# Performance work log

Measured on AMD Instinct MI355X. Metric: run time of the kernel, lower is better.

## Reference

```python
import jax, jax.numpy as jnp
import numpy as np

MIN = 1e-15   # norm / denominator clamp (as in Poincare ball impl)
EPS = 1e-7    # artanh input clamp (fp32-safe version of 1-1e-15)
C = 1.0       # curvature (c_in == c_out == 1.0)
B, N, D = 1, 1024, 64


def _artanh(y):
    y = jnp.clip(y, -1.0 + EPS, 1.0 - EPS)
    return 0.5 * (jnp.log1p(y) - jnp.log1p(-y))


def _norm(v):
    return jnp.maximum(jnp.linalg.norm(v, axis=-1, keepdims=True), MIN)


def expmap0(u, c):
    sqc = jnp.sqrt(c)
    n = _norm(u)
    return jnp.tanh(sqc * n) * u / (sqc * n)


def logmap0(p, c):
    sqc = jnp.sqrt(c)
    n = _norm(p)
    return _artanh(sqc * n) * p / (sqc * n)


def mobius_add(x, y, c):
    x2 = jnp.sum(x * x, -1, keepdims=True)
    y2 = jnp.sum(y * y, -1, keepdims=True)
    xy = jnp.sum(x * y, -1, keepdims=True)
    num = (1.0 + 2.0 * c * xy + c * y2) * x + (1.0 - c * x2) * y
    den = 1.0 + 2.0 * c * xy + c * c * x2 * y2
    return num / jnp.maximum(den, MIN)


def mobius_matvec(m, x, c):
    # m: [out, in], x: [B, N, in]
    sqc = jnp.sqrt(c)
    xn = _norm(x)
    mx = jnp.einsum('bnd,ed->bne', x, m)
    mxn = _norm(mx)
    res = jnp.tanh(mxn / xn * _artanh(sqc * xn)) * mx / (mxn * sqc)
    cond = jnp.all(mx == 0.0, axis=-1, keepdims=True)
    return jnp.where(cond, jnp.zeros_like(res), res)


def logmap(p1, p2, c):
    # tangent vector at p1 pointing to p2 (broadcasts)
    sqc = jnp.sqrt(c)
    sub = mobius_add(-p1, p2, c)
    sn = _norm(sub)
    lam = 2.0 / jnp.maximum(1.0 - c * jnp.sum(p1 * p1, -1, keepdims=True), MIN)
    return 2.0 / (sqc * lam) * _artanh(sqc * sn) * sub / sn


def expmap(u, p, c):
    # exp map of tangent u at point p (call order matches torch code: expmap(x, support_t))
    sqc = jnp.sqrt(c)
    un = _norm(u)
    lam = 2.0 / jnp.maximum(1.0 - c * jnp.sum(p * p, -1, keepdims=True), MIN)
    second = jnp.tanh(sqc / 2.0 * lam * un) * u / (sqc * un)
    return mobius_add(p, second, c)


def setup_inputs() -> dict:
    key = jax.random.key(0)
    k1, k2, k3, k4, k5 = jax.random.split(key, 5)
    # hyperbolic points: expmap0 of small tangent vectors -> valid Poincare-ball points
    x = expmap0(0.1 * jax.random.normal(k1, (B, N, D), jnp.float32), C)
    adj = (jax.random.uniform(k2, (B, N, N)) < 0.05).astype(jnp.float32)
    # xavier_uniform with gain sqrt(2): bound = sqrt(2)*sqrt(6/(D+D))
    bound = np.sqrt(2.0) * np.sqrt(6.0 / (D + D))
    weight = jax.random.uniform(k3, (D, D), jnp.float32, -bound, bound)
    bias = 0.01 * jax.random.normal(k4, (D,), jnp.float32)
    kw, kb = jax.random.split(k5)
    ab = np.sqrt(6.0 / (2 * D + 1))
    att_w = jax.random.uniform(kw, (1, 2 * D), jnp.float32, -ab, ab)
    att_b = 0.01 * jax.random.normal(kb, (1,), jnp.float32)
    return {"x": x, "adj": adj, "weight": weight, "bias": bias,
            "att_w": att_w, "att_b": att_b}


def reference(x, adj, weight, bias, att_w, att_b):
    c = C
    # ---- HypLinear (dropout=0 / eval mode) ----
    h = mobius_matvec(weight, x, c)
    hyp_bias = expmap0(bias[None, :], c)          # proj_tan0 is identity on the ball
    h = mobius_add(h, hyp_bias, c)                # [B,N,D]
    # ---- HypAgg: use_att + local_agg ----
    h_tan = logmap0(h, c)                         # [B,N,D]
    # pairwise logmap: tangent_i[j] = logmap(h_i, h_j)  -> [B,N,N,D]
    local_tan = logmap(h[:, :, None, :], h[:, None, :, :], c)
    # DenseAtt on tangent features
    left = jnp.broadcast_to(h_tan[:, :, None, :], (B, N, N, D))
    right = jnp.broadcast_to(h_tan[:, None, :, :], (B, N, N, D))
    cat = jnp.concatenate([left, right], axis=-1)          # [B,N,N,2D]
    logits = jnp.einsum('bijk,ok->bij', cat, att_w) + att_b[0]
    att = jax.nn.sigmoid(logits) * adj                     # [B,N,N]
    support = jnp.sum(att[..., None] * local_tan, axis=2)  # [B,N,D]
    out = expmap(h, support, c)                            # faithful arg order: (x, support_t)
    # ---- HypAct ----
    t = jax.nn.relu(logmap0(out, c))
    return expmap0(t, c)
```

## Files before the change

### kernel.cpp

```cpp
#include <hip/hip_runtime.h>
#include <hip/hip_bf16.h>

#define NODES 1024
#define DIM   64
#define MINV  1e-15f
#define EPSV  1e-7f
#define WPAD  66
#define HPAD  66
#define CH    64

__device__ __forceinline__ float artanh_f(float y) {
    y = fminf(fmaxf(y, -1.f + EPSV), 1.f - EPSV);
    return 0.5f * (log1pf(y) - log1pf(-y));
}

__device__ __forceinline__ float waveReduceSum(float v) {
#pragma unroll
    for (int m = 1; m < 64; m <<= 1) v += __shfl_xor(v, m, 64);
    return v;
}

__global__ __launch_bounds__(256) void prep_kernel(
    const float* __restrict__ x,
    const float* __restrict__ weight,
    const float* __restrict__ bias,
    const float* __restrict__ att_w,
    float* __restrict__ H, float* __restrict__ X2,
    float* __restrict__ L, float* __restrict__ R)
{
    __shared__ float sx[4][DIM];
    __shared__ float Wl[DIM][WPAD];
    const int tid = threadIdx.x;
    const int wv  = tid >> 6;
    const int t   = tid & 63;
    const int i   = blockIdx.x * 4 + wv;

#pragma unroll
    for (int p = 0; p < 4; ++p) {
        const int k = p * 1024 + tid * 4;
        const float4 w4 = *reinterpret_cast<const float4*>(weight + k);
        const int r = k >> 6, c = k & 63;
        Wl[r][c + 0] = w4.x; Wl[r][c + 1] = w4.y;
        Wl[r][c + 2] = w4.z; Wl[r][c + 3] = w4.w;
    }

    const float xd = x[i * DIM + t];
    sx[wv][t] = xd;
    __syncthreads();

    const float xn = fmaxf(sqrtf(waveReduceSum(xd * xd)), MINV);

    float mx = 0.f;
    const float* sxr = sx[wv];
#pragma unroll
    for (int d = 0; d < DIM; d += 2) {
        const float2 w2 = *reinterpret_cast<const float2*>(&Wl[t][d]);
        mx = fmaf(sxr[d + 0], w2.x, mx);
        mx = fmaf(sxr[d + 1], w2.y, mx);
    }

    const float mxn = fmaxf(sqrtf(waveReduceSum(mx * mx)), MINV);
    const float res = tanhf(mxn / xn * artanh_f(xn)) * mx / mxn;

    const float bd = bias[t];
    const float bn = fmaxf(sqrtf(waveReduceSum(bd * bd)), MINV);
    const float hb = tanhf(bn) * bd / bn;

    const float y2  = waveReduceSum(hb * hb);
    const float x2r = waveReduceSum(res * res);
    const float xy  = waveReduceSum(res * hb);
    const float num = (1.f + 2.f * xy + y2) * res + (1.f - x2r) * hb;
    const float den = fmaxf(1.f + 2.f * xy + x2r * y2, MINV);
    const float h   = num / den;

    const float x2 = waveReduceSum(h * h);
    H[i * DIM + t] = h;

    const float n  = fmaxf(sqrtf(x2), MINV);
    const float ht = artanh_f(n) / n * h;
    const float Li = waveReduceSum(ht * att_w[t]);
    const float Ri = waveReduceSum(ht * att_w[DIM + t]);

    if (t == 0) { X2[i] = x2; L[i] = Li; R[i] = Ri; }
}

__global__ __launch_bounds__(256) void agg_kernel(
    const float* __restrict__ H, const float* __restrict__ X2,
    const float* __restrict__ L, const float* __restrict__ R,
    const float* __restrict__ adj,
    const float* __restrict__ att_b,
    float* __restrict__ out)
{
    __shared__ float shi[DIM];
    __shared__ float Hl[CH][HPAD];
    __shared__ float f_arr[CH];
    __shared__ int   slist[NODES];
    __shared__ int   wbase[4];
    __shared__ float svred[4][DIM];
    __shared__ float s0red[4];

    const int i   = blockIdx.x;
    const int tid = threadIdx.x;
    const int wv  = tid >> 6;
    const int ln  = tid & 63;
    const int grp = tid >> 4;
    const int gl  = tid & 15;
    const int d0  = gl * 4;

    if (tid < DIM) shi[tid] = H[i * DIM + tid];

    const float4 a4 = *reinterpret_cast<const float4*>(adj + i * NODES + tid * 4);
    const int c0 = (a4.x != 0.f), c1 = (a4.y != 0.f), c2 = (a4.z != 0.f), c3 = (a4.w != 0.f);
    const int cntv = c0 + c1 + c2 + c3;

    int pfx = cntv;
#pragma unroll
    for (int d = 1; d < 64; d <<= 1) {
        const int tsh = __shfl_up(pfx, d, 64);
        if (ln >= d) pfx += tsh;
    }
    if (ln == 63) wbase[wv] = pfx;
    __syncthreads();

    int base = 0;
#pragma unroll
    for (int w = 0; w < 4; ++w) if (w < wv) base += wbase[w];
    int pos = base + pfx - cntv;
    const int j0 = tid * 4;
    if (c0) slist[pos++] = j0 + 0;
    if (c1) slist[pos++] = j0 + 1;
    if (c2) slist[pos++] = j0 + 2;
    if (c3) slist[pos++] = j0 + 3;
    __syncthreads();
    const int cnt = wbase[0] + wbase[1] + wbase[2] + wbase[3];

    const float x2i   = X2[i];
    const float Li    = L[i];
    const float Bi    = 1.f - x2i;
    const float coefi = fmaxf(Bi, MINV);
    const float attb  = att_b[0];

    float4 vacc = make_float4(0.f, 0.f, 0.f, 0.f);
    float  s0   = 0.f;

    for (int cb = 0; cb < cnt; cb += CH) {
        const int m = min(CH, cnt - cb);

        {
            const int il = tid >> 4;
#pragma unroll
            for (int p = 0; p < 4; ++p) {
                const int ii = il + p * 16;
                if (ii < m) {
                    const int j = slist[cb + ii];
                    const float4 hv = *reinterpret_cast<const float4*>(H + j * DIM + d0);
                    float* dst = &Hl[ii][d0];
                    dst[0] = hv.x; dst[1] = hv.y; dst[2] = hv.z; dst[3] = hv.w;
                }
            }
        }
        __syncthreads();

        if (tid < m) {
            const int j = slist[cb + tid];
            float dot = 0.f;
            const float* hr = Hl[tid];
#pragma unroll
            for (int d = 0; d < DIM; d += 2) {
                const float2 h2 = *reinterpret_cast<const float2*>(&hr[d]);
                dot = fmaf(shi[d + 0], h2.x, dot);
                dot = fmaf(shi[d + 1], h2.y, dot);
            }

            const float y2  = X2[j];
            const float A   = 1.f - 2.f * dot + y2;
            const float den = fmaxf(1.f - 2.f * dot + x2i * y2, MINV);
            const float q   = fmaxf(A * A * x2i - 2.f * A * Bi * dot + Bi * Bi * y2, 0.f);
            const float sn  = fmaxf(sqrtf(q) / den, MINV);
            const float ratio = artanh_f(sn) / sn;

            const float logit = Li + R[j] + attb;
            const float sig   = 1.f / (1.f + expf(-logit));
            const float f     = sig * coefi * ratio / den;

            f_arr[tid] = f;
            s0 += f * A;
        }
        __syncthreads();

        for (int il = grp; il < m; il += 16) {
            const float fv = f_arr[il];
            const float* hr = &Hl[il][d0];
            vacc.x = fmaf(fv, hr[0], vacc.x);
            vacc.y = fmaf(fv, hr[1], vacc.y);
            vacc.z = fmaf(fv, hr[2], vacc.z);
            vacc.w = fmaf(fv, hr[3], vacc.w);
        }
        __syncthreads();
    }

    vacc.x += __shfl_xor(vacc.x, 16, 64); vacc.x += __shfl_xor(vacc.x, 32, 64);
    vacc.y += __shfl_xor(vacc.y, 16, 64); vacc.y += __shfl_xor(vacc.y, 32, 64);
    vacc.z += __shfl_xor(vacc.z, 16, 64); vacc.z += __shfl_xor(vacc.z, 32, 64);
    vacc.w += __shfl_xor(vacc.w, 16, 64); vacc.w += __shfl_xor(vacc.w, 32, 64);
    s0 = waveReduceSum(s0);

    if (ln < 16) {
        svred[wv][ln * 4 + 0] = vacc.x;
        svred[wv][ln * 4 + 1] = vacc.y;
        svred[wv][ln * 4 + 2] = vacc.z;
        svred[wv][ln * 4 + 3] = vacc.w;
    }
    if (ln == 0) s0red[wv] = s0;
    __syncthreads();

    if (tid < DIM) {
        const float svec = svred[0][tid] + svred[1][tid] + svred[2][tid] + svred[3][tid];
        const float s0t  = s0red[0] + s0red[1] + s0red[2] + s0red[3];
        const float hd   = shi[tid];
        const float sup  = -s0t * hd + Bi * svec;

        const float s2     = waveReduceSum(sup * sup);
        const float coef_s = fmaxf(1.f - s2, MINV);
        const float un     = fmaxf(sqrtf(x2i), MINV);
        const float tt     = tanhf(un / coef_s);
        const float sec    = tt * hd / un;

        const float y2s = waveReduceSum(sec * sec);
        const float xy  = waveReduceSum(sup * sec);
        const float num = (1.f + 2.f * xy + y2s) * sup + (1.f - s2) * sec;
        const float den = fmaxf(1.f + 2.f * xy + s2 * y2s, MINV);
        const float od  = num / den;

        const float on   = fmaxf(sqrtf(waveReduceSum(od * od)), MINV);
        const float tanv = artanh_f(on) / on * od;
        const float tv   = fmaxf(tanv, 0.f);
        const float tn   = fmaxf(sqrtf(waveReduceSum(tv * tv)), MINV);
        const float fin  = tanhf(tn) / tn * tv;

        out[i * DIM + tid] = fin;
    }
}

extern "C" void kernel_launch(void* const* d_in, const int* in_sizes, int n_in,
                              void* d_out, int out_size, void* d_ws, size_t ws_size,
                              hipStream_t stream) {
    const float* x      = (const float*)d_in[0];
    const float* adj    = (const float*)d_in[1];
    const float* weight = (const float*)d_in[2];
    const float* bias   = (const float*)d_in[3];
    const float* att_w  = (const float*)d_in[4];
    const float* att_b  = (const float*)d_in[5];

    float* ws = (float*)d_ws;
    float* H  = ws;
    float* X2 = ws + NODES * DIM;
    float* Lb = X2 + NODES;
    float* Rb = Lb + NODES;

    prep_kernel<<<NODES / 4, 256, 0, stream>>>(x, weight, bias, att_w, H, X2, Lb, Rb);
    agg_kernel<<<NODES, 256, 0, stream>>>(H, X2, Lb, Rb, adj, att_b,
                                          (float*)d_out);
}
```

Baseline: 18.58 us.

## Restructure aggregation kernel as single-wave blocks without LDS tiling

```diff
diff --git a/kernel.cpp b/kernel.cpp
--- a/kernel.cpp
+++ b/kernel.cpp
@@ -6,8 +6,6 @@
 #define MINV  1e-15f
 #define EPSV  1e-7f
 #define WPAD  66
-#define HPAD  66
-#define CH    64
 
 __device__ __forceinline__ float artanh_f(float y) {
     y = fminf(fmaxf(y, -1.f + EPSV), 1.f - EPSV);
@@ -18,6 +16,15 @@
 #pragma unroll
     for (int m = 1; m < 64; m <<= 1) v += __shfl_xor(v, m, 64);
     return v;
+}
+
+__device__ __forceinline__ void waveReduceSum2(float& a, float& b) {
+#pragma unroll
+    for (int m = 1; m < 64; m <<= 1) {
+        const float ta = __shfl_xor(a, m, 64);
+        const float tb = __shfl_xor(b, m, 64);
+        a += ta; b += tb;
+    }
 }
 
 __global__ __launch_bounds__(256) void prep_kernel(
@@ -84,55 +91,49 @@
     if (t == 0) { X2[i] = x2; L[i] = Li; R[i] = Ri; }
 }
 
-__global__ __launch_bounds__(256) void agg_kernel(
+__global__ __launch_bounds__(64) void agg_kernel(
     const float* __restrict__ H, const float* __restrict__ X2,
     const float* __restrict__ L, const float* __restrict__ R,
     const float* __restrict__ adj,
     const float* __restrict__ att_b,
     float* __restrict__ out)
 {
-    __shared__ float shi[DIM];
-    __shared__ float Hl[CH][HPAD];
-    __shared__ float f_arr[CH];
+    __shared__ float sh[DIM];
+    __shared__ float f_arr[NODES];
     __shared__ int   slist[NODES];
-    __shared__ int   wbase[4];
-    __shared__ float svred[4][DIM];
-    __shared__ float s0red[4];
-
-    const int i   = blockIdx.x;
-    const int tid = threadIdx.x;
-    const int wv  = tid >> 6;
-    const int ln  = tid & 63;
-    const int grp = tid >> 4;
-    const int gl  = tid & 15;
-    const int d0  = gl * 4;
-
-    if (tid < DIM) shi[tid] = H[i * DIM + tid];
-
-    const float4 a4 = *reinterpret_cast<const float4*>(adj + i * NODES + tid * 4);
-    const int c0 = (a4.x != 0.f), c1 = (a4.y != 0.f), c2 = (a4.z != 0.f), c3 = (a4.w != 0.f);
-    const int cntv = c0 + c1 + c2 + c3;
-
+
+    const int i  = blockIdx.x;
+    const int ln = threadIdx.x;
+
+    const float hd = H[i * DIM + ln];
+    sh[ln] = hd;
+
+    unsigned m16 = 0;
+    {
+        const float4* arow = reinterpret_cast<const float4*>(adj + i * NODES + ln * 16);
+#pragma unroll
+        for (int q = 0; q < 4; ++q) {
+            const float4 a = arow[q];
+            m16 |= (a.x != 0.f ? 1u : 0u) << (q * 4 + 0);
+            m16 |= (a.y != 0.f ? 1u : 0u) << (q * 4 + 1);
+            m16 |= (a.z != 0.f ? 1u : 0u) << (q * 4 + 2);
+            m16 |= (a.w != 0.f ? 1u : 0u) << (q * 4 + 3);
+        }
+    }
+    const int cntv = __popc(m16);
     int pfx = cntv;
 #pragma unroll
     for (int d = 1; d < 64; d <<= 1) {
-        const int tsh = __shfl_up(pfx, d, 64);
-        if (ln >= d) pfx += tsh;
-    }
-    if (ln == 63) wbase[wv] = pfx;
+        const int t = __shfl_up(pfx, d, 64);
+        if (ln >= d) pfx += t;
+    }
+    const int cnt = __shfl(pfx, 63, 64);
+    int pos = pfx - cntv;
+    const int jb = ln * 16;
+#pragma unroll
+    for (int q = 0; q < 16; ++q)
+        if (m16 & (1u << q)) slist[pos++] = jb + q;
     __syncthreads();
-
-    int base = 0;
-#pragma unroll
-    for (int w = 0; w < 4; ++w) if (w < wv) base += wbase[w];
-    int pos = base + pfx - cntv;
-    const int j0 = tid * 4;
-    if (c0) slist[pos++] = j0 + 0;
-    if (c1) slist[pos++] = j0 + 1;
-    if (c2) slist[pos++] = j0 + 2;
-    if (c3) slist[pos++] = j0 + 3;
-    __syncthreads();
-    const int cnt = wbase[0] + wbase[1] + wbase[2] + wbase[3];
 
     const float x2i   = X2[i];
     const float Li    = L[i];
@@ -140,106 +141,69 @@
     const float coefi = fmaxf(Bi, MINV);
     const float attb  = att_b[0];
 
-    float4 vacc = make_float4(0.f, 0.f, 0.f, 0.f);
-    float  s0   = 0.f;
-
-    for (int cb = 0; cb < cnt; cb += CH) {
-        const int m = min(CH, cnt - cb);
-
-        {
-            const int il = tid >> 4;
-#pragma unroll
-            for (int p = 0; p < 4; ++p) {
-                const int ii = il + p * 16;
-                if (ii < m) {
-                    const int j = slist[cb + ii];
-                    const float4 hv = *reinterpret_cast<const float4*>(H + j * DIM + d0);
-                    float* dst = &Hl[ii][d0];
-                    dst[0] = hv.x; dst[1] = hv.y; dst[2] = hv.z; dst[3] = hv.w;
-                }
-            }
+    float s0 = 0.f;
+    for (int k = ln; k < cnt; k += 64) {
+        const int j  = slist[k];
+        const float y2 = X2[j];
+        const float Rj = R[j];
+
+        float dot = 0.f;
+        const float* hj = H + j * DIM;
+#pragma unroll
+        for (int dd = 0; dd < DIM; dd += 4) {
+            const float4 h4 = *reinterpret_cast<const float4*>(hj + dd);
+            const float4 s4 = *reinterpret_cast<const float4*>(&sh[dd]);
+            dot = fmaf(h4.x, s4.x, dot);
+            dot = fmaf(h4.y, s4.y, dot);
+            dot = fmaf(h4.z, s4.z, dot);
+            dot = fmaf(h4.w, s4.w, dot);
         }
-        __syncthreads();
-
-        if (tid < m) {
-            const int j = slist[cb + tid];
-            float dot = 0.f;
-            const float* hr = Hl[tid];
-#pragma unroll
-            for (int d = 0; d < DIM; d += 2) {
-                const float2 h2 = *reinterpret_cast<const float2*>(&hr[d]);
-                dot = fmaf(shi[d + 0], h2.x, dot);
-                dot = fmaf(shi[d + 1], h2.y, dot);
-            }
-
-            const float y2  = X2[j];
-            const float A   = 1.f - 2.f * dot + y2;
-            const float den = fmaxf(1.f - 2.f * dot + x2i * y2, MINV);
-            const float q   = fmaxf(A * A * x2i - 2.f * A * Bi * dot + Bi * Bi * y2, 0.f);
-            const float sn  = fmaxf(sqrtf(q) / den, MINV);
-            const float ratio = artanh_f(sn) / sn;
-
-            const float logit = Li + R[j] + attb;
-            const float sig   = 1.f / (1.f + expf(-logit));
-            const float f     = sig * coefi * ratio / den;
-
-            f_arr[tid] = f;
-            s0 += f * A;
-        }
-        __syncthreads();
-
-        for (int il = grp; il < m; il += 16) {
-            const float fv = f_arr[il];
-            const float* hr = &Hl[il][d0];
-            vacc.x = fmaf(fv, hr[0], vacc.x);
-            vacc.y = fmaf(fv, hr[1], vacc.y);
-            vacc.z = fmaf(fv, hr[2], vacc.z);
-            vacc.w = fmaf(fv, hr[3], vacc.w);
-        }
-        __syncthreads();
-    }
-
-    vacc.x += __shfl_xor(vacc.x, 16, 64); vacc.x += __shfl_xor(vacc.x, 32, 64);
-    vacc.y += __shfl_xor(vacc.y, 16, 64); vacc.y += __shfl_xor(vacc.y, 32, 64);
-    vacc.z += __shfl_xor(vacc.z, 16, 64); vacc.z += __shfl_xor(vacc.z, 32, 64);
-    vacc.w += __shfl_xor(vacc.w, 16, 64); vacc.w += __shfl_xor(vacc.w, 32, 64);
+
+        const float A   = 1.f - 2.f * dot + y2;
+        const float den = fmaxf(1.f - 2.f * dot + x2i * y2, MINV);
+        const float q   = fmaxf(A * A * x2i - 2.f * A * Bi * dot + Bi * Bi * y2, 0.f);
+        const float sn  = fmaxf(sqrtf(q) / den, MINV);
+        const float ratio = artanh_f(sn) / sn;
+
+        const float sig = 1.f / (1.f + expf(-(Li + Rj + attb)));
+        const float f   = sig * coefi * ratio / den;
+
+        f_arr[k] = f;
+        s0 += f * A;
+    }
+    __syncthreads();
+
+    float sv = 0.f;
+#pragma unroll 4
+    for (int k = 0; k < cnt; ++k) {
+        const int j   = slist[k];
+        const float f = f_arr[k];
+        sv = fmaf(f, H[j * DIM + ln], sv);
+    }
+
     s0 = waveReduceSum(s0);
-
-    if (ln < 16) {
-        svred[wv][ln * 4 + 0] = vacc.x;
-        svred[wv][ln * 4 + 1] = vacc.y;
-        svred[wv][ln * 4 + 2] = vacc.z;
-        svred[wv][ln * 4 + 3] = vacc.w;
-    }
-    if (ln == 0) s0red[wv] = s0;
-    __syncthreads();
-
-    if (tid < DIM) {
-        const float svec = svred[0][tid] + svred[1][tid] + svred[2][tid] + svred[3][tid];
-        const float s0t  = s0red[0] + s0red[1] + s0red[2] + s0red[3];
-        const float hd   = shi[tid];
-        const float sup  = -s0t * hd + Bi * svec;
-
-        const float s2     = waveReduceSum(sup * sup);
-        const float coef_s = fmaxf(1.f - s2, MINV);
-        const float un     = fmaxf(sqrtf(x2i), MINV);
-        const float tt     = tanhf(un / coef_s);
-        const float sec    = tt * hd / un;
-
-        const float y2s = waveReduceSum(sec * sec);
-        const float xy  = waveReduceSum(sup * sec);
-        const float num = (1.f + 2.f * xy + y2s) * sup + (1.f - s2) * sec;
-        const float den = fmaxf(1.f + 2.f * xy + s2 * y2s, MINV);
-        const float od  = num / den;
-
-        const float on   = fmaxf(sqrtf(waveReduceSum(od * od)), MINV);
-        const float tanv = artanh_f(on) / on * od;
-        const float tv   = fmaxf(tanv, 0.f);
-        const float tn   = fmaxf(sqrtf(waveReduceSum(tv * tv)), MINV);
-        const float fin  = tanhf(tn) / tn * tv;
-
-        out[i * DIM + tid] = fin;
-    }
+    const float sup = -s0 * hd + Bi * sv;
+
+    const float s2     = waveReduceSum(sup * sup);
+    const float coef_s = fmaxf(1.f - s2, MINV);
+    const float un     = fmaxf(sqrtf(x2i), MINV);
+    const float tt     = tanhf(un / coef_s);
+    const float sec    = tt * hd / un;
+
+    float y2s = sec * sec;
+    float xy  = sup * sec;
+    waveReduceSum2(y2s, xy);
+    const float num = (1.f + 2.f * xy + y2s) * sup + (1.f - s2) * sec;
+    const float den = fmaxf(1.f + 2.f * xy + s2 * y2s, MINV);
+    const float od  = num / den;
+
+    const float on   = fmaxf(sqrtf(waveReduceSum(od * od)), MINV);
+    const float tanv = artanh_f(on) / on * od;
+    const float tv   = fmaxf(tanv, 0.f);
+    const float tn   = fmaxf(sqrtf(waveReduceSum(tv * tv)), MINV);
+    const float fin  = tanhf(tn) / tn * tv;
+
+    out[i * DIM + ln] = fin;
 }
 
 extern "C" void kernel_launch(void* const* d_in, const int* in_sizes, int n_in,
@@ -259,6 +223,6 @@
     float* Rb = Lb + NODES;
 
     prep_kernel<<<NODES / 4, 256, 0, stream>>>(x, weight, bias, att_w, H, X2, Lb, Rb);
-    agg_kernel<<<NODES, 256, 0, stream>>>(H, X2, Lb, Rb, adj, att_b,
-                                          (float*)d_out);
-}
+    agg_kernel<<<NODES, 64, 0, stream>>>(H, X2, Lb, Rb, adj, att_b,
+                                         (float*)d_out);
+}
```

Result: slower. 20.81 us (+12.0%).

## Fuse prep and aggregation kernels with a software grid barrier

Applied to the files above, without the earlier changes.

```diff
diff --git a/kernel.cpp b/kernel.cpp
--- a/kernel.cpp
+++ b/kernel.cpp
@@ -8,6 +8,7 @@
 #define WPAD  66
 #define HPAD  66
 #define CH    64
+#define GRID  256
 
 __device__ __forceinline__ float artanh_f(float y) {
     y = fminf(fmaxf(y, -1.f + EPSV), 1.f - EPSV);
@@ -19,78 +20,38 @@
     for (int m = 1; m < 64; m <<= 1) v += __shfl_xor(v, m, 64);
     return v;
 }
-
-__global__ __launch_bounds__(256) void prep_kernel(
+__device__ __forceinline__ void waveReduceSum2(float& a, float& b) {
+#pragma unroll
+    for (int m = 1; m < 64; m <<= 1) {
+        const float ta = __shfl_xor(a, m, 64);
+        const float tb = __shfl_xor(b, m, 64);
+        a += ta; b += tb;
+    }
+}
+__device__ __forceinline__ void waveReduceSum3(float& a, float& b, float& c) {
+#pragma unroll
+    for (int m = 1; m < 64; m <<= 1) {
+        const float ta = __shfl_xor(a, m, 64);
+        const float tb = __shfl_xor(b, m, 64);
+        const float tc = __shfl_xor(c, m, 64);
+        a += ta; b += tb; c += tc;
+    }
+}
+
+__global__ __launch_bounds__(256) void fused_kernel(
     const float* __restrict__ x,
+    const float* __restrict__ adj,
     const float* __restrict__ weight,
     const float* __restrict__ bias,
     const float* __restrict__ att_w,
+    const float* __restrict__ att_b,
     float* __restrict__ H, float* __restrict__ X2,
-    float* __restrict__ L, float* __restrict__ R)
+    float* __restrict__ L, float* __restrict__ R,
+    unsigned* __restrict__ bar,
+    float* __restrict__ out)
 {
     __shared__ float sx[4][DIM];
     __shared__ float Wl[DIM][WPAD];
-    const int tid = threadIdx.x;
-    const int wv  = tid >> 6;
-    const int t   = tid & 63;
-    const int i   = blockIdx.x * 4 + wv;
-
-#pragma unroll
-    for (int p = 0; p < 4; ++p) {
-        const int k = p * 1024 + tid * 4;
-        const float4 w4 = *reinterpret_cast<const float4*>(weight + k);
-        const int r = k >> 6, c = k & 63;
-        Wl[r][c + 0] = w4.x; Wl[r][c + 1] = w4.y;
-        Wl[r][c + 2] = w4.z; Wl[r][c + 3] = w4.w;
-    }
-
-    const float xd = x[i * DIM + t];
-    sx[wv][t] = xd;
-    __syncthreads();
-
-    const float xn = fmaxf(sqrtf(waveReduceSum(xd * xd)), MINV);
-
-    float mx = 0.f;
-    const float* sxr = sx[wv];
-#pragma unroll
-    for (int d = 0; d < DIM; d += 2) {
-        const float2 w2 = *reinterpret_cast<const float2*>(&Wl[t][d]);
-        mx = fmaf(sxr[d + 0], w2.x, mx);
-        mx = fmaf(sxr[d + 1], w2.y, mx);
-    }
-
-    const float mxn = fmaxf(sqrtf(waveReduceSum(mx * mx)), MINV);
-    const float res = tanhf(mxn / xn * artanh_f(xn)) * mx / mxn;
-
-    const float bd = bias[t];
-    const float bn = fmaxf(sqrtf(waveReduceSum(bd * bd)), MINV);
-    const float hb = tanhf(bn) * bd / bn;
-
-    const float y2  = waveReduceSum(hb * hb);
-    const float x2r = waveReduceSum(res * res);
-    const float xy  = waveReduceSum(res * hb);
-    const float num = (1.f + 2.f * xy + y2) * res + (1.f - x2r) * hb;
-    const float den = fmaxf(1.f + 2.f * xy + x2r * y2, MINV);
-    const float h   = num / den;
-
-    const float x2 = waveReduceSum(h * h);
-    H[i * DIM + t] = h;
-
-    const float n  = fmaxf(sqrtf(x2), MINV);
-    const float ht = artanh_f(n) / n * h;
-    const float Li = waveReduceSum(ht * att_w[t]);
-    const float Ri = waveReduceSum(ht * att_w[DIM + t]);
-
-    if (t == 0) { X2[i] = x2; L[i] = Li; R[i] = Ri; }
-}
-
-__global__ __launch_bounds__(256) void agg_kernel(
-    const float* __restrict__ H, const float* __restrict__ X2,
-    const float* __restrict__ L, const float* __restrict__ R,
-    const float* __restrict__ adj,
-    const float* __restrict__ att_b,
-    float* __restrict__ out)
-{
     __shared__ float shi[DIM];
     __shared__ float Hl[CH][HPAD];
     __shared__ float f_arr[CH];
@@ -99,146 +60,213 @@
     __shared__ float svred[4][DIM];
     __shared__ float s0red[4];
 
-    const int i   = blockIdx.x;
     const int tid = threadIdx.x;
     const int wv  = tid >> 6;
-    const int ln  = tid & 63;
+    const int t   = tid & 63;
+
+    {
+        const int i = blockIdx.x * 4 + wv;
+
+#pragma unroll
+        for (int p = 0; p < 4; ++p) {
+            const int k = p * 1024 + tid * 4;
+            const float4 w4 = *reinterpret_cast<const float4*>(weight + k);
+            const int r = k >> 6, c = k & 63;
+            Wl[r][c + 0] = w4.x; Wl[r][c + 1] = w4.y;
+            Wl[r][c + 2] = w4.z; Wl[r][c + 3] = w4.w;
+        }
+
+        const float xd = x[i * DIM + t];
+        sx[wv][t] = xd;
+        __syncthreads();
+
+        const float xn = fmaxf(sqrtf(waveReduceSum(xd * xd)), MINV);
+
+        float mx = 0.f;
+        const float* sxr = sx[wv];
+#pragma unroll
+        for (int d = 0; d < DIM; d += 2) {
+            const float2 w2 = *reinterpret_cast<const float2*>(&Wl[t][d]);
+            mx = fmaf(sxr[d + 0], w2.x, mx);
+            mx = fmaf(sxr[d + 1], w2.y, mx);
+        }
+
+        const float bd = bias[t];
+        float mxn2 = mx * mx, bn2 = bd * bd;
+        waveReduceSum2(mxn2, bn2);
+        const float mxn = fmaxf(sqrtf(mxn2), MINV);
+        const float res = tanhf(mxn / xn * artanh_f(xn)) * mx / mxn;
+        const float bn  = fmaxf(sqrtf(bn2), MINV);
+        const float hb  = tanhf(bn) * bd / bn;
+
+        float y2 = hb * hb, x2r = res * res, xy = res * hb;
+        waveReduceSum3(y2, x2r, xy);
+        const float num = (1.f + 2.f * xy + y2) * res + (1.f - x2r) * hb;
+        const float den = fmaxf(1.f + 2.f * xy + x2r * y2, MINV);
+        const float h   = num / den;
+
+        const float x2 = waveReduceSum(h * h);
+        H[i * DIM + t] = h;
+
+        const float n  = fmaxf(sqrtf(x2), MINV);
+        const float ht = artanh_f(n) / n * h;
+        float Li = ht * att_w[t], Ri = ht * att_w[DIM + t];
+        waveReduceSum2(Li, Ri);
+
+        if (t == 0) { X2[i] = x2; L[i] = Li; R[i] = Ri; }
+    }
+
+    __syncthreads();
+    if (tid == 0) {
+        __threadfence();
+        atomicAdd(bar, 1u);
+        unsigned spins = 0;
+        while (atomicAdd(bar, 0u) < GRID && ++spins < 100000000u)
+            __builtin_amdgcn_s_sleep(2);
+        __threadfence();
+    }
+    __syncthreads();
+
     const int grp = tid >> 4;
     const int gl  = tid & 15;
     const int d0  = gl * 4;
-
-    if (tid < DIM) shi[tid] = H[i * DIM + tid];
-
-    const float4 a4 = *reinterpret_cast<const float4*>(adj + i * NODES + tid * 4);
-    const int c0 = (a4.x != 0.f), c1 = (a4.y != 0.f), c2 = (a4.z != 0.f), c3 = (a4.w != 0.f);
-    const int cntv = c0 + c1 + c2 + c3;
-
-    int pfx = cntv;
-#pragma unroll
-    for (int d = 1; d < 64; d <<= 1) {
-        const int tsh = __shfl_up(pfx, d, 64);
-        if (ln >= d) pfx += tsh;
-    }
-    if (ln == 63) wbase[wv] = pfx;
-    __syncthreads();
-
-    int base = 0;
-#pragma unroll
-    for (int w = 0; w < 4; ++w) if (w < wv) base += wbase[w];
-    int pos = base + pfx - cntv;
-    const int j0 = tid * 4;
-    if (c0) slist[pos++] = j0 + 0;
-    if (c1) slist[pos++] = j0 + 1;
-    if (c2) slist[pos++] = j0 + 2;
-    if (c3) slist[pos++] = j0 + 3;
-    __syncthreads();
-    const int cnt = wbase[0] + wbase[1] + wbase[2] + wbase[3];
-
-    const float x2i   = X2[i];
-    const float Li    = L[i];
-    const float Bi    = 1.f - x2i;
-    const float coefi = fmaxf(Bi, MINV);
-    const float attb  = att_b[0];
-
-    float4 vacc = make_float4(0.f, 0.f, 0.f, 0.f);
-    float  s0   = 0.f;
-
-    for (int cb = 0; cb < cnt; cb += CH) {
-        const int m = min(CH, cnt - cb);
-
-        {
-            const int il = tid >> 4;
-#pragma unroll
-            for (int p = 0; p < 4; ++p) {
-                const int ii = il + p * 16;
-                if (ii < m) {
-                    const int j = slist[cb + ii];
-                    const float4 hv = *reinterpret_cast<const float4*>(H + j * DIM + d0);
-                    float* dst = &Hl[ii][d0];
-                    dst[0] = hv.x; dst[1] = hv.y; dst[2] = hv.z; dst[3] = hv.w;
+    const float attb = att_b[0];
+
+    for (int r = 0; r < 4; ++r) {
+        const int i = blockIdx.x * 4 + r;
+        __syncthreads();
+
+        if (tid < DIM) shi[tid] = H[i * DIM + tid];
+
+        const float4 a4 = *reinterpret_cast<const float4*>(adj + i * NODES + tid * 4);
+        const int c0 = (a4.x != 0.f), c1 = (a4.y != 0.f), c2 = (a4.z != 0.f), c3 = (a4.w != 0.f);
+        const int cntv = c0 + c1 + c2 + c3;
+
+        int pfx = cntv;
+#pragma unroll
+        for (int d = 1; d < 64; d <<= 1) {
+            const int tsh = __shfl_up(pfx, d, 64);
+            if (t >= d) pfx += tsh;
+        }
+        if (t == 63) wbase[wv] = pfx;
+        __syncthreads();
+
+        int base = 0;
+#pragma unroll
+        for (int w = 0; w < 4; ++w) if (w < wv) base += wbase[w];
+        int pos = base + pfx - cntv;
+        const int j0 = tid * 4;
+        if (c0) slist[pos++] = j0 + 0;
+        if (c1) slist[pos++] = j0 + 1;
+        if (c2) slist[pos++] = j0 + 2;
+        if (c3) slist[pos++] = j0 + 3;
+        __syncthreads();
+        const int cnt = wbase[0] + wbase[1] + wbase[2] + wbase[3];
+
+        const float x2i   = X2[i];
+        const float Li    = L[i];
+        const float Bi    = 1.f - x2i;
+        const float coefi = fmaxf(Bi, MINV);
+
+        float4 vacc = make_float4(0.f, 0.f, 0.f, 0.f);
+        float  s0   = 0.f;
+
+        for (int cb = 0; cb < cnt; cb += CH) {
+            const int m = min(CH, cnt - cb);
+
+            {
+                const int il = tid >> 4;
+#pragma unroll
+                for (int p = 0; p < 4; ++p) {
+                    const int ii = il + p * 16;
+                    if (ii < m) {
+                        const int j = slist[cb + ii];
+                        const float4 hv = *reinterpret_cast<const float4*>(H + j * DIM + d0);
+                        float* dst = &Hl[ii][d0];
+                        dst[0] = hv.x; dst[1] = hv.y; dst[2] = hv.z; dst[3] = hv.w;
+                    }
                 }
             }
-        }
-        __syncthreads();
-
-        if (tid < m) {
-            const int j = slist[cb + tid];
-            float dot = 0.f;
-            const float* hr = Hl[tid];
-#pragma unroll
-            for (int d = 0; d < DIM; d += 2) {
-                const float2 h2 = *reinterpret_cast<const float2*>(&hr[d]);
-                dot = fmaf(shi[d + 0], h2.x, dot);
-                dot = fmaf(shi[d + 1], h2.y, dot);
+            __syncthreads();
+
+            if (tid < m) {
+                const int j = slist[cb + tid];
+                float dot = 0.f;
+                const float* hr = Hl[tid];
+#pragma unroll
+                for (int d = 0; d < DIM; d += 2) {
+                    const float2 h2 = *reinterpret_cast<const float2*>(&hr[d]);
+                    dot = fmaf(shi[d + 0], h2.x, dot);
+                    dot = fmaf(shi[d + 1], h2.y, dot);
+                }
+
+                const float y2  = X2[j];
+                const float A   = 1.f - 2.f * dot + y2;
+                const float den = fmaxf(1.f - 2.f * dot + x2i * y2, MINV);
+                const float q   = fmaxf(A * A * x2i - 2.f * A * Bi * dot + Bi * Bi * y2, 0.f);
+                const float sn  = fmaxf(sqrtf(q) / den, MINV);
+                const float ratio = artanh_f(sn) / sn;
+
+                const float sig = 1.f / (1.f + expf(-(Li + R[j] + attb)));
+                const float f   = sig * coefi * ratio / den;
+
+                f_arr[tid] = f;
+                s0 += f * A;
             }
-
-            const float y2  = X2[j];
-            const float A   = 1.f - 2.f * dot + y2;
-            const float den = fmaxf(1.f - 2.f * dot + x2i * y2, MINV);
-            const float q   = fmaxf(A * A * x2i - 2.f * A * Bi * dot + Bi * Bi * y2, 0.f);
-            const float sn  = fmaxf(sqrtf(q) / den, MINV);
-            const float ratio = artanh_f(sn) / sn;
-
-            const float logit = Li + R[j] + attb;
-            const float sig   = 1.f / (1.f + expf(-logit));
-            const float f     = sig * coefi * ratio / den;
-
-            f_arr[tid] = f;
-            s0 += f * A;
-        }
-        __syncthreads();
-
-        for (int il = grp; il < m; il += 16) {
-            const float fv = f_arr[il];
-            const float* hr = &Hl[il][d0];
-            vacc.x = fmaf(fv, hr[0], vacc.x);
-            vacc.y = fmaf(fv, hr[1], vacc.y);
-            vacc.z = fmaf(fv, hr[2], vacc.z);
-            vacc.w = fmaf(fv, hr[3], vacc.w);
-        }
-        __syncthreads();
-    }
-
-    vacc.x += __shfl_xor(vacc.x, 16, 64); vacc.x += __shfl_xor(vacc.x, 32, 64);
-    vacc.y += __shfl_xor(vacc.y, 16, 64); vacc.y += __shfl_xor(vacc.y, 32, 64);
-    vacc.z += __shfl_xor(vacc.z, 16, 64); vacc.z += __shfl_xor(vacc.z, 32, 64);
-    vacc.w += __shfl_xor(vacc.w, 16, 64); vacc.w += __shfl_xor(vacc.w, 32, 64);
-    s0 = waveReduceSum(s0);
-
-    if (ln < 16) {
-        svred[wv][ln * 4 + 0] = vacc.x;
-        svred[wv][ln * 4 + 1] = vacc.y;
-        svred[wv][ln * 4 + 2] = vacc.z;
-        svred[wv][ln * 4 + 3] = vacc.w;
-    }
-    if (ln == 0) s0red[wv] = s0;
-    __syncthreads();
-
-    if (tid < DIM) {
-        const float svec = svred[0][tid] + svred[1][tid] + svred[2][tid] + svred[3][tid];
-        const float s0t  = s0red[0] + s0red[1] + s0red[2] + s0red[3];
-        const float hd   = shi[tid];
-        const float sup  = -s0t * hd + Bi * svec;
-
-        const float s2     = waveReduceSum(sup * sup);
-        const float coef_s = fmaxf(1.f - s2, MINV);
-        const float un     = fmaxf(sqrtf(x2i), MINV);
-        const float tt     = tanhf(un / coef_s);
-        const float sec    = tt * hd / un;
-
-        const float y2s = waveReduceSum(sec * sec);
-        const float xy  = waveReduceSum(sup * sec);
-        const float num = (1.f + 2.f * xy + y2s) * sup + (1.f - s2) * sec;
-        const float den = fmaxf(1.f + 2.f * xy + s2 * y2s, MINV);
-        const float od  = num / den;
-
-        const float on   = fmaxf(sqrtf(waveReduceSum(od * od)), MINV);
-        const float tanv = artanh_f(on) / on * od;
-        const float tv   = fmaxf(tanv, 0.f);
-        const float tn   = fmaxf(sqrtf(waveReduceSum(tv * tv)), MINV);
-        const float fin  = tanhf(tn) / tn * tv;
-
-        out[i * DIM + tid] = fin;
+            __syncthreads();
+
+            for (int il = grp; il < m; il += 16) {
+                const float fv = f_arr[il];
+                const float* hr = &Hl[il][d0];
+                vacc.x = fmaf(fv, hr[0], vacc.x);
+                vacc.y = fmaf(fv, hr[1], vacc.y);
+                vacc.z = fmaf(fv, hr[2], vacc.z);
+                vacc.w = fmaf(fv, hr[3], vacc.w);
+            }
+            __syncthreads();
+        }
+
+        vacc.x += __shfl_xor(vacc.x, 16, 64); vacc.x += __shfl_xor(vacc.x, 32, 64);
+        vacc.y += __shfl_xor(vacc.y, 16, 64); vacc.y += __shfl_xor(vacc.y, 32, 64);
+        vacc.z += __shfl_xor(vacc.z, 16, 64); vacc.z += __shfl_xor(vacc.z, 32, 64);
+        vacc.w += __shfl_xor(vacc.w, 16, 64); vacc.w += __shfl_xor(vacc.w, 32, 64);
+        s0 = waveReduceSum(s0);
+
+        if (t < 16) {
+            svred[wv][t * 4 + 0] = vacc.x;
+            svred[wv][t * 4 + 1] = vacc.y;
+            svred[wv][t * 4 + 2] = vacc.z;
+            svred[wv][t * 4 + 3] = vacc.w;
+        }
+        if (t == 0) s0red[wv] = s0;
+        __syncthreads();
+
+        if (tid < DIM) {
+            const float svec = svred[0][tid] + svred[1][tid] + svred[2][tid] + svred[3][tid];
+            const float s0t  = s0red[0] + s0red[1] + s0red[2] + s0red[3];
+            const float hd   = shi[tid];
+            const float sup  = -s0t * hd + Bi * svec;
+
+            const float s2     = waveReduceSum(sup * sup);
+            const float coef_s = fmaxf(1.f - s2, MINV);
+            const float un     = fmaxf(sqrtf(x2i), MINV);
+            const float tt     = tanhf(un / coef_s);
+            const float sec    = tt * hd / un;
+
+            float y2s = sec * sec, xy = sup * sec;
+            waveReduceSum2(y2s, xy);
+            const float num = (1.f + 2.f * xy + y2s) * sup + (1.f - s2) * sec;
+            const float den = fmaxf(1.f + 2.f * xy + s2 * y2s, MINV);
+            const float od  = num / den;
+
+            const float on   = fmaxf(sqrtf(waveReduceSum(od * od)), MINV);
+            const float tanv = artanh_f(on) / on * od;
+            const float tv   = fmaxf(tanv, 0.f);
+            const float tn   = fmaxf(sqrtf(waveReduceSum(tv * tv)), MINV);
+            const float fin  = tanhf(tn) / tn * tv;
+
+            out[i * DIM + tid] = fin;
+        }
     }
 }
 
@@ -253,12 +281,13 @@
     const float* att_b  = (const float*)d_in[5];
 
     float* ws = (float*)d_ws;
-    float* H  = ws;
-    float* X2 = ws + NODES * DIM;
-    float* Lb = X2 + NODES;
-    float* Rb = Lb + NODES;
-
-    prep_kernel<<<NODES / 4, 256, 0, stream>>>(x, weight, bias, att_w, H, X2, Lb, Rb);
-    agg_kernel<<<NODES, 256, 0, stream>>>(H, X2, Lb, Rb, adj, att_b,
-                                          (float*)d_out);
-}
+    float*    H   = ws;
+    float*    X2  = ws + NODES * DIM;
+    float*    Lb  = X2 + NODES;
+    float*    Rb  = Lb + NODES;
+    unsigned* bar = (unsigned*)(Rb + NODES);
+
+    hipMemsetAsync(bar, 0, sizeof(unsigned), stream);
+    fused_kernel<<<GRID, 256, 0, stream>>>(x, adj, weight, bias, att_w, att_b,
+                                           H, X2, Lb, Rb, bar, (float*)d_out);
+}
```

After: 53.97 us. +190.4%, slower.
